# Kernel optimization log

Measured on AMD Instinct MI355X. Metric: run time of the kernel, lower is better.

## Reference

```python
import jax, jax.numpy as jnp
import numpy as np

N, E, R = 50000, 500000, 3
IN, HID, OUT = 128, 128, 128
NEG_SLOPE = 0.2


def setup_inputs() -> dict:
    key = jax.random.key(0)
    ks = jax.random.split(key, 16)
    g = lambda i, shape: jax.random.normal(ks[i], shape, jnp.float32) * 0.1
    return {
        "x": jax.random.normal(ks[0], (N, IN), jnp.float32),
        "edge_index": jax.random.randint(ks[1], (2, E), 0, N, jnp.int32),
        "edge_type": jax.random.randint(ks[2], (E,), 0, R, jnp.int32),
        "edge_attr": jax.random.normal(ks[3], (E, 1), jnp.float32),
        # conv1 params (RGATConv: per-relation weight, q/k/e attention vectors, edge lin, bias)
        "w1": g(4, (R, IN, HID)), "q1": g(5, (HID, 1)), "k1": g(6, (HID, 1)),
        "le1": g(7, (1, HID)), "e1": g(8, (HID, 1)), "b1": jnp.zeros((HID,), jnp.float32),
        # conv2 params
        "w2": g(9, (R, HID, OUT)), "q2": g(10, (OUT, 1)), "k2": g(11, (OUT, 1)),
        "le2": g(12, (1, OUT)), "e2": g(13, (OUT, 1)), "b2": jnp.zeros((OUT,), jnp.float32),
    }


def _rgat_conv(x, src, dst, edge_type, edge_attr, w, q, k, le, e, b):
    """PyG RGATConv: heads=1, dim=1, additive-self-attention, across-relation softmax."""
    n = x.shape[0]
    # Per-relation linear at node level (equiv. to per-edge bmm with w[edge_type])
    xw = jnp.einsum('ni,rio->rno', x, w)            # [R, N, C]
    x_j = xw[edge_type, src]                          # [E, C] transformed source feats
    x_i = xw[edge_type, dst]                          # [E, C] transformed target feats
    # additive attention logits: q(x_i) + k(x_j) + e(lin_edge(edge_attr))
    alpha = x_i @ q + x_j @ k + (edge_attr @ le) @ e  # [E, 1]
    alpha = jax.nn.leaky_relu(alpha, negative_slope=NEG_SLOPE)
    # across-relation softmax over incoming edges of each target node
    amax = jax.ops.segment_max(alpha, dst, num_segments=n)
    amax = jnp.where(jnp.isfinite(amax), amax, 0.0)   # empty segments -> 0
    ex = jnp.exp(alpha - amax[dst])
    denom = jax.ops.segment_sum(ex, dst, num_segments=n)
    alpha = ex / (denom[dst] + 1e-16)
    # weighted scatter-add aggregation, then bias (concat=True, heads=1)
    out = jax.ops.segment_sum(alpha * x_j, dst, num_segments=n)  # [N, C]
    return out + b


def reference(x, edge_index, edge_type, edge_attr,
              w1, q1, k1, le1, e1, b1,
              w2, q2, k2, le2, e2, b2):
    src, dst = edge_index[0], edge_index[1]
    h = jax.nn.relu(_rgat_conv(x, src, dst, edge_type, edge_attr, w1, q1, k1, le1, e1, b1))
    return _rgat_conv(h, src, dst, edge_type, edge_attr, w2, q2, k2, le2, e2, b2)
```

## Files before the change

### kernel.cpp

```cpp
#include <hip/hip_runtime.h>
#include <hip/hip_bf16.h>
#include <math.h>

typedef __bf16 bf16x8 __attribute__((ext_vector_type(8)));
typedef float f32x4 __attribute__((ext_vector_type(4)));

#define CDIM 128

__global__ void sentinel_kernel(float* outf) {
  if (threadIdx.x == 0) outf[0] = 12345.0f;
}

__global__ __launch_bounds__(256) void prep_kernel(
    const float* __restrict__ w1, const float* __restrict__ w2,
    __hip_bfloat16* __restrict__ wt,
    const float* __restrict__ le1, const float* __restrict__ e1,
    const float* __restrict__ le2, const float* __restrict__ e2,
    float* __restrict__ outc, int* __restrict__ deg, int perW, int n) {
  const int b = blockIdx.x;
  const int tid = threadIdx.x;
  if (b < 48) {
    int t = b * 256 + tid;
    if (t >= perW * 2) return;
    const float* w = (t < perW) ? w1 : w2;
    int tt = (t < perW) ? t : t - perW;
    int r = tt >> 11;
    int rem = tt & 2047;
    int kb = rem >> 7;
    int o = rem & 127;
    const float* wr = w + ((size_t)r << 14);
    union { __hip_bfloat16 h[8]; int4 v; } u;
#pragma unroll
    for (int j = 0; j < 8; ++j)
      u.h[j] = __float2bfloat16(wr[(size_t)(kb * 8 + j) * CDIM + o]);
    *reinterpret_cast<int4*>(wt + (size_t)t * 8) = u.v;
  } else if (b == 48) {
    if (tid < 64) {
      float v1 = le1[tid] * e1[tid] + le1[tid + 64] * e1[tid + 64];
      float v2 = le2[tid] * e2[tid] + le2[tid + 64] * e2[tid + 64];
#pragma unroll
      for (int off = 32; off > 0; off >>= 1) {
        v1 += __shfl_xor(v1, off, 64);
        v2 += __shfl_xor(v2, off, 64);
      }
      if (tid == 0) { outc[0] = v1; outc[1] = v2; }
    }
  } else {
    int i = (b - 49) * 256 + tid;
    if (i < n) deg[i] = 0;
  }
}


__global__ __launch_bounds__(256) void hist_kernel(const int* __restrict__ dstv,
                                                   int* __restrict__ deg, int E) {
  int e = blockIdx.x * 256 + threadIdx.x;
  if (e < E) atomicAdd(&deg[dstv[e]], 1);
}

__global__ __launch_bounds__(256) void scan1_kernel(const int* __restrict__ deg,
                                                    int* __restrict__ rowptr,
                                                    int* __restrict__ partials, int n) {
  __shared__ int sh[256];
  int t = threadIdx.x;
  int base = blockIdx.x * 1024;
  int idx = base + t * 4;
  int v[4]; int s = 0;
#pragma unroll
  for (int j = 0; j < 4; ++j) { v[j] = (idx + j < n) ? deg[idx + j] : 0; s += v[j]; }
  sh[t] = s;
  __syncthreads();
  for (int off = 1; off < 256; off <<= 1) {
    int x = (t >= off) ? sh[t - off] : 0;
    __syncthreads();
    sh[t] += x;
    __syncthreads();
  }
  int excl = sh[t] - s;
  if (t == 255) partials[blockIdx.x] = sh[255];
  int run = excl;
#pragma unroll
  for (int j = 0; j < 4; ++j) {
    if (idx + j < n) rowptr[idx + j] = run;
    run += v[j];
  }
}

__global__ __launch_bounds__(256) void scan2_kernel(int* __restrict__ partials, int nb) {
  __shared__ int sh[256];
  int t = threadIdx.x;
  int v = (t < nb) ? partials[t] : 0;
  sh[t] = v;
  __syncthreads();
  for (int off = 1; off < 256; off <<= 1) {
    int x = (t >= off) ? sh[t - off] : 0;
    __syncthreads();
    sh[t] += x;
    __syncthreads();
  }
  if (t < nb) partials[t] = sh[t] - v;
}

__global__ __launch_bounds__(256) void scan3_kernel(int* __restrict__ rowptr,
                                                    int* __restrict__ cursor,
                                                    const int* __restrict__ partials,
                                                    int n, int E) {
  int i = blockIdx.x * 256 + threadIdx.x;
  if (i < n) {
    int v = rowptr[i] + partials[i >> 10];
    rowptr[i] = v;
    cursor[i] = v;
  } else if (i == n) {
    rowptr[n] = E;
  }
}

__global__ __launch_bounds__(256) void scatter_kernel(
    const int* __restrict__ srcv, const int* __restrict__ dstv,
    const int* __restrict__ etype, const float* __restrict__ eattr,
    int* __restrict__ cursor, int2* __restrict__ kattr, int E, int n) {
  int e = blockIdx.x * 256 + threadIdx.x;
  if (e >= E) return;
  int p = atomicAdd(&cursor[dstv[e]], 1);
  kattr[p] = make_int2(etype[e] * n + srcv[e], __float_as_int(eattr[e]));
}

__global__ __launch_bounds__(256) void gemm_xw_kernel(
    const float* __restrict__ xin, const __hip_bfloat16* __restrict__ wt,
    const float* __restrict__ qv, const float* __restrict__ kv,
    __hip_bfloat16* __restrict__ xwout, float* __restrict__ sq, float* __restrict__ sk,
    int n) {
  __shared__ __hip_bfloat16 wlds[16 * 128 * 8];
  __shared__ float qls[128], kls[128];
  const int base = blockIdx.x * 128;
  const int tid = threadIdx.x;
  const int wave = tid >> 6, lane = tid & 63;
  const int quad = lane >> 4, c16 = lane & 15;

  if (tid < 128) qls[tid] = qv[tid];
  else kls[tid - 128] = kv[tid - 128];

  bf16x8 zf;
#pragma unroll
  for (int j = 0; j < 8; ++j) zf[j] = (__bf16)0.0f;

  bf16x8 af[2][4];
#pragma unroll
  for (int h = 0; h < 2; ++h) {
    int m = base + wave * 32 + h * 16 + c16;
#pragma unroll
    for (int ks = 0; ks < 4; ++ks) {
      if (m < n) {
        const float* xp = xin + (size_t)m * CDIM + ks * 32 + quad * 8;
        f32x4 x0 = *reinterpret_cast<const f32x4*>(xp);
        f32x4 x1 = *reinterpret_cast<const f32x4*>(xp + 4);
        bf16x8 a;
#pragma unroll
        for (int j = 0; j < 4; ++j) { a[j] = (__bf16)x0[j]; a[4 + j] = (__bf16)x1[j]; }
        af[h][ks] = a;
      } else {
        af[h][ks] = zf;
      }
    }
  }

  for (int r = 0; r < 3; ++r) {
    if (r) __syncthreads();
    {
      const int4* src = reinterpret_cast<const int4*>(wt + ((size_t)r << 14));
      int4* dst = reinterpret_cast<int4*>(wlds);
      for (int i = tid; i < 2048; i += 256) dst[i] = src[i];
    }
    __syncthreads();

    f32x4 acc[2][8];
#pragma unroll
    for (int h = 0; h < 2; ++h)
#pragma unroll
      for (int ot = 0; ot < 8; ++ot) acc[h][ot] = (f32x4){0.f, 0.f, 0.f, 0.f};

#pragma unroll
    for (int ks = 0; ks < 4; ++ks) {
#pragma unroll
      for (int ot = 0; ot < 8; ++ot) {
        bf16x8 b = *reinterpret_cast<const bf16x8*>(
            &wlds[(((ks * 4 + quad) * 128) + ot * 16 + c16) * 8]);
        acc[0][ot] = __builtin_amdgcn_mfma_f32_16x16x32_bf16(b, af[0][ks], acc[0][ot], 0, 0, 0);
        acc[1][ot] = __builtin_amdgcn_mfma_f32_16x16x32_bf16(b, af[1][ks], acc[1][ot], 0, 0, 0);
      }
    }

#pragma unroll
    for (int h = 0; h < 2; ++h) {
      const int grow = base + wave * 32 + h * 16 + c16;
      const bool ok = grow < n;
      __hip_bfloat16* rp = xwout + (((size_t)r * n + grow) << 7) + quad * 4;
      float s_q = 0.f, s_k = 0.f;
#pragma unroll
      for (int ot = 0; ot < 8; ++ot) {
        f32x4 a = acc[h][ot];
        f32x4 q4 = *reinterpret_cast<const f32x4*>(&qls[ot * 16 + quad * 4]);
        f32x4 k4 = *reinterpret_cast<const f32x4*>(&kls[ot * 16 + quad * 4]);
        s_q += a[0] * q4[0] + a[1] * q4[1] + a[2] * q4[2] + a[3] * q4[3];
        s_k += a[0] * k4[0] + a[1] * k4[1] + a[2] * k4[2] + a[3] * k4[3];
        if (ok) {
          union { __hip_bfloat16 b4[4]; uint2 u; } pk;
#pragma unroll
          for (int t = 0; t < 4; ++t) pk.b4[t] = __float2bfloat16(a[t]);
          *reinterpret_cast<uint2*>(rp + ot * 16) = pk.u;
        }
      }
      s_q += __shfl_xor(s_q, 16, 64);
      s_q += __shfl_xor(s_q, 32, 64);
      s_k += __shfl_xor(s_k, 16, 64);
      s_k += __shfl_xor(s_k, 32, 64);
      if (quad == 0 && ok) {
        sq[(size_t)r * n + grow] = s_q;
        sk[(size_t)r * n + grow] = s_k;
      }
    }
  }
}

__global__ __launch_bounds__(256) void aggregate_kernel(
    const int* __restrict__ rowptr, const int2* __restrict__ kattr,
    const float* __restrict__ sq, const float* __restrict__ sk,
    const __hip_bfloat16* __restrict__ xw, const float* __restrict__ bias,
    const float* __restrict__ cscal, float* __restrict__ out, int n, int do_relu) {
  const int wave = threadIdx.x >> 6, lane = threadIdx.x & 63;
  const int node = blockIdx.x * 4 + wave;
  if (node >= n) return;
  const int g = lane >> 4;
  const int sub = lane & 15;
  const float c = cscal[0];
  const int n2 = n * 2;

  const int start = rowptr[node];
  const int deg = rowptr[node + 1] - start;
  const float s0 = sq[node], s1 = sq[n + node], s2 = sq[n2 + node];

  float acc[8];
#pragma unroll
  for (int t = 0; t < 8; ++t) acc[t] = 0.f;
  float den = 0.f;

  for (int j0 = 0; j0 < deg; j0 += 8) {
    const int j = j0 + (g << 1);
    const bool v0 = j < deg, v1 = j + 1 < deg;
    int2 ka0 = kattr[start + (v0 ? j : 0)];
    int2 ka1 = kattr[start + (v1 ? j + 1 : 0)];
    int kk0 = ka0.x, kk1 = ka1.x;
    float l0 = (kk0 >= n2 ? s2 : (kk0 >= n ? s1 : s0)) + sk[kk0] + c * __int_as_float(ka0.y);
    float l1 = (kk1 >= n2 ? s2 : (kk1 >= n ? s1 : s0)) + sk[kk1] + c * __int_as_float(ka1.y);
    l0 = l0 > 0.f ? l0 : 0.2f * l0;
    l1 = l1 > 0.f ? l1 : 0.2f * l1;
    float w0 = v0 ? __expf(l0) : 0.f;
    float w1 = v1 ? __expf(l1) : 0.f;
    bf16x8 f0 = *reinterpret_cast<const bf16x8*>(xw + ((size_t)kk0 << 7) + sub * 8);
    bf16x8 f1 = *reinterpret_cast<const bf16x8*>(xw + ((size_t)kk1 << 7) + sub * 8);
#pragma unroll
    for (int t = 0; t < 8; ++t) acc[t] += w0 * (float)f0[t] + w1 * (float)f1[t];
    den += w0 + w1;
  }

#pragma unroll
  for (int t = 0; t < 8; ++t) {
    acc[t] += __shfl_xor(acc[t], 16, 64);
    acc[t] += __shfl_xor(acc[t], 32, 64);
  }
  den += __shfl_xor(den, 16, 64);
  den += __shfl_xor(den, 32, 64);

  if (g == 0) {
    float inv = 1.0f / (den + 1e-16f);
    f32x4 b0 = *reinterpret_cast<const f32x4*>(bias + sub * 8);
    f32x4 b1 = *reinterpret_cast<const f32x4*>(bias + sub * 8 + 4);
    f32x4 o0, o1;
#pragma unroll
    for (int t = 0; t < 4; ++t) {
      o0[t] = acc[t] * inv + b0[t];
      o1[t] = acc[4 + t] * inv + b1[t];
    }
    if (do_relu) {
#pragma unroll
      for (int t = 0; t < 4; ++t) {
        o0[t] = fmaxf(o0[t], 0.f);
        o1[t] = fmaxf(o1[t], 0.f);
      }
    }
    float* op = out + (size_t)node * CDIM + sub * 8;
    *reinterpret_cast<f32x4*>(op) = o0;
    *reinterpret_cast<f32x4*>(op + 4) = o1;
  }
}


extern "C" void kernel_launch(void* const* d_in, const int* in_sizes, int n_in,
                              void* d_out, int out_size, void* d_ws, size_t ws_size,
                              hipStream_t stream) {
  const float* x     = (const float*)d_in[0];
  const int*   eidx  = (const int*)d_in[1];
  const int*   etype = (const int*)d_in[2];
  const float* eattr = (const float*)d_in[3];
  const float* w1  = (const float*)d_in[4];
  const float* q1  = (const float*)d_in[5];
  const float* k1  = (const float*)d_in[6];
  const float* le1 = (const float*)d_in[7];
  const float* e1  = (const float*)d_in[8];
  const float* b1  = (const float*)d_in[9];
  const float* w2  = (const float*)d_in[10];
  const float* q2  = (const float*)d_in[11];
  const float* k2  = (const float*)d_in[12];
  const float* le2 = (const float*)d_in[13];
  const float* e2  = (const float*)d_in[14];
  const float* b2  = (const float*)d_in[15];

  const int N = in_sizes[0] / CDIM;
  const int E = in_sizes[2];
  const int R = in_sizes[4] / (CDIM * CDIM);
  const int* srcv = eidx;
  const int* dstv = eidx + E;

  char* p = (char*)d_ws;
  auto alloc = [&](size_t bytes) -> void* {
    void* q = (void*)p;
    p += (bytes + 255) & ~(size_t)255;
    return q;
  };
  float* sq       = (float*)alloc((size_t)R * N * 4);
  float* sk       = (float*)alloc((size_t)R * N * 4);
  int*   deg      = (int*)alloc((size_t)N * 4);
  int*   rowptr   = (int*)alloc((size_t)(N + 1) * 4);
  int*   cursor   = (int*)alloc((size_t)N * 4);
  int*   partials = (int*)alloc(4096);
  int2*  kattr    = (int2*)alloc((size_t)E * 8);
  __hip_bfloat16* wt = (__hip_bfloat16*)alloc((size_t)2 * R * CDIM * CDIM * 2);
  float* cscal    = (float*)alloc(256);
  __hip_bfloat16* xw = (__hip_bfloat16*)alloc((size_t)R * N * CDIM * 2);

  size_t needed = (size_t)(p - (char*)d_ws);
  if (needed > ws_size) {
    sentinel_kernel<<<1, 64, 0, stream>>>((float*)d_out);
    return;
  }

  float* outp = (float*)d_out;
  float* hbuf = outp;

  const int eg = (E + 255) / 256;
  const int nb = (N + 1023) / 1024;
  const int nodes4 = (N + 3) / 4;
  const int perW = R * 2048;
  const int prep_grid = 49 + (N + 255) / 256;

  prep_kernel<<<prep_grid, 256, 0, stream>>>(w1, w2, wt, le1, e1, le2, e2,
                                             cscal, deg, perW, N);

  hist_kernel<<<eg, 256, 0, stream>>>(dstv, deg, E);
  scan1_kernel<<<nb, 256, 0, stream>>>(deg, rowptr, partials, N);
  scan2_kernel<<<1, 256, 0, stream>>>(partials, nb);
  scan3_kernel<<<(N + 1 + 255) / 256, 256, 0, stream>>>(rowptr, cursor, partials, N, E);
  scatter_kernel<<<eg, 256, 0, stream>>>(srcv, dstv, etype, eattr, cursor, kattr, E, N);

  dim3 ggrid((N + 127) / 128);

  gemm_xw_kernel<<<ggrid, 256, 0, stream>>>(x, wt, q1, k1, xw, sq, sk, N);
  aggregate_kernel<<<nodes4, 256, 0, stream>>>(rowptr, kattr, sq, sk, xw, b1,
                                               cscal + 0, hbuf, N, 1);

  gemm_xw_kernel<<<ggrid, 256, 0, stream>>>(hbuf, wt + (size_t)R * CDIM * CDIM,
                                            q2, k2, xw, sq, sk, N);
  aggregate_kernel<<<nodes4, 256, 0, stream>>>(rowptr, kattr, sq, sk, xw, b2,
                                               cscal + 1, outp, N, 0);
}
```

Before: 263.1 us.

## Fold scan2 into scan3, halve GEMM rows per block, unroll aggregate gather 4x

Three separate changes. The second-level prefix scan is folded into scan3 as a per-block wavefront shuffle scan over the partials, which removes one kernel launch. The xW GEMM now gives each block 64 rows instead of 128, with one 16-row tile per wave. This doubles the grid and cuts accumulator registers, at the cost of reloading the weight tiles into LDS twice as often overall. The aggregation loop now has each 16-lane group handle 4 edges per iteration instead of 2, so more independent gathers are in flight. That comes with higher register use and more wasted lanes on low-degree nodes.

```diff
diff --git a/kernel.cpp b/kernel.cpp
--- a/kernel.cpp
+++ b/kernel.cpp
@@ -86,28 +86,26 @@
   }
 }
 
-__global__ __launch_bounds__(256) void scan2_kernel(int* __restrict__ partials, int nb) {
-  __shared__ int sh[256];
-  int t = threadIdx.x;
-  int v = (t < nb) ? partials[t] : 0;
-  sh[t] = v;
-  __syncthreads();
-  for (int off = 1; off < 256; off <<= 1) {
-    int x = (t >= off) ? sh[t - off] : 0;
-    __syncthreads();
-    sh[t] += x;
-    __syncthreads();
-  }
-  if (t < nb) partials[t] = sh[t] - v;
-}
-
 __global__ __launch_bounds__(256) void scan3_kernel(int* __restrict__ rowptr,
                                                     int* __restrict__ cursor,
                                                     const int* __restrict__ partials,
-                                                    int n, int E) {
-  int i = blockIdx.x * 256 + threadIdx.x;
+                                                    int nb, int n, int E) {
+  __shared__ int spfx[64];
+  int t = threadIdx.x;
+  if (t < 64) {
+    int pv = (t < nb) ? partials[t] : 0;
+    int v = pv;
+#pragma unroll
+    for (int off = 1; off < 64; off <<= 1) {
+      int u = __shfl_up(v, off, 64);
+      if (t >= off) v += u;
+    }
+    spfx[t] = v - pv;
+  }
+  __syncthreads();
+  int i = blockIdx.x * 256 + t;
   if (i < n) {
-    int v = rowptr[i] + partials[i >> 10];
+    int v = rowptr[i] + spfx[i >> 10];
     rowptr[i] = v;
     cursor[i] = v;
   } else if (i == n) {
@@ -132,7 +130,7 @@
     int n) {
   __shared__ __hip_bfloat16 wlds[16 * 128 * 8];
   __shared__ float qls[128], kls[128];
-  const int base = blockIdx.x * 128;
+  const int base = blockIdx.x * 64;
   const int tid = threadIdx.x;
   const int wave = tid >> 6, lane = tid & 63;
   const int quad = lane >> 4, c16 = lane & 15;
@@ -144,23 +142,21 @@
 #pragma unroll
   for (int j = 0; j < 8; ++j) zf[j] = (__bf16)0.0f;
 
-  bf16x8 af[2][4];
-#pragma unroll
-  for (int h = 0; h < 2; ++h) {
-    int m = base + wave * 32 + h * 16 + c16;
-#pragma unroll
-    for (int ks = 0; ks < 4; ++ks) {
-      if (m < n) {
-        const float* xp = xin + (size_t)m * CDIM + ks * 32 + quad * 8;
-        f32x4 x0 = *reinterpret_cast<const f32x4*>(xp);
-        f32x4 x1 = *reinterpret_cast<const f32x4*>(xp + 4);
-        bf16x8 a;
-#pragma unroll
-        for (int j = 0; j < 4; ++j) { a[j] = (__bf16)x0[j]; a[4 + j] = (__bf16)x1[j]; }
-        af[h][ks] = a;
-      } else {
-        af[h][ks] = zf;
-      }
+  const int m = base + wave * 16 + c16;
+  const bool ok = m < n;
+  bf16x8 af[4];
+#pragma unroll
+  for (int ks = 0; ks < 4; ++ks) {
+    if (ok) {
+      const float* xp = xin + (size_t)m * CDIM + ks * 32 + quad * 8;
+      f32x4 x0 = *reinterpret_cast<const f32x4*>(xp);
+      f32x4 x1 = *reinterpret_cast<const f32x4*>(xp + 4);
+      bf16x8 a;
+#pragma unroll
+      for (int j = 0; j < 4; ++j) { a[j] = (__bf16)x0[j]; a[4 + j] = (__bf16)x1[j]; }
+      af[ks] = a;
+    } else {
+      af[ks] = zf;
     }
   }
 
@@ -169,15 +165,14 @@
     {
       const int4* src = reinterpret_cast<const int4*>(wt + ((size_t)r << 14));
       int4* dst = reinterpret_cast<int4*>(wlds);
-      for (int i = tid; i < 2048; i += 256) dst[i] = src[i];
+#pragma unroll
+      for (int i = 0; i < 8; ++i) dst[tid + i * 256] = src[tid + i * 256];
     }
     __syncthreads();
 
-    f32x4 acc[2][8];
-#pragma unroll
-    for (int h = 0; h < 2; ++h)
-#pragma unroll
-      for (int ot = 0; ot < 8; ++ot) acc[h][ot] = (f32x4){0.f, 0.f, 0.f, 0.f};
+    f32x4 acc[8];
+#pragma unroll
+    for (int ot = 0; ot < 8; ++ot) acc[ot] = (f32x4){0.f, 0.f, 0.f, 0.f};
 
 #pragma unroll
     for (int ks = 0; ks < 4; ++ks) {
@@ -185,39 +180,33 @@
       for (int ot = 0; ot < 8; ++ot) {
         bf16x8 b = *reinterpret_cast<const bf16x8*>(
             &wlds[(((ks * 4 + quad) * 128) + ot * 16 + c16) * 8]);
-        acc[0][ot] = __builtin_amdgcn_mfma_f32_16x16x32_bf16(b, af[0][ks], acc[0][ot], 0, 0, 0);
-        acc[1][ot] = __builtin_amdgcn_mfma_f32_16x16x32_bf16(b, af[1][ks], acc[1][ot], 0, 0, 0);
+        acc[ot] = __builtin_amdgcn_mfma_f32_16x16x32_bf16(b, af[ks], acc[ot], 0, 0, 0);
       }
     }
 
-#pragma unroll
-    for (int h = 0; h < 2; ++h) {
-      const int grow = base + wave * 32 + h * 16 + c16;
-      const bool ok = grow < n;
-      __hip_bfloat16* rp = xwout + (((size_t)r * n + grow) << 7) + quad * 4;
-      float s_q = 0.f, s_k = 0.f;
-#pragma unroll
-      for (int ot = 0; ot < 8; ++ot) {
-        f32x4 a = acc[h][ot];
-        f32x4 q4 = *reinterpret_cast<const f32x4*>(&qls[ot * 16 + quad * 4]);
-        f32x4 k4 = *reinterpret_cast<const f32x4*>(&kls[ot * 16 + quad * 4]);
-        s_q += a[0] * q4[0] + a[1] * q4[1] + a[2] * q4[2] + a[3] * q4[3];
-        s_k += a[0] * k4[0] + a[1] * k4[1] + a[2] * k4[2] + a[3] * k4[3];
-        if (ok) {
-          union { __hip_bfloat16 b4[4]; uint2 u; } pk;
-#pragma unroll
-          for (int t = 0; t < 4; ++t) pk.b4[t] = __float2bfloat16(a[t]);
-          *reinterpret_cast<uint2*>(rp + ot * 16) = pk.u;
-        }
+    __hip_bfloat16* rp = xwout + (((size_t)r * n + m) << 7) + quad * 4;
+    float s_q = 0.f, s_k = 0.f;
+#pragma unroll
+    for (int ot = 0; ot < 8; ++ot) {
+      f32x4 a = acc[ot];
+      f32x4 q4 = *reinterpret_cast<const f32x4*>(&qls[ot * 16 + quad * 4]);
+      f32x4 k4 = *reinterpret_cast<const f32x4*>(&kls[ot * 16 + quad * 4]);
+      s_q += a[0] * q4[0] + a[1] * q4[1] + a[2] * q4[2] + a[3] * q4[3];
+      s_k += a[0] * k4[0] + a[1] * k4[1] + a[2] * k4[2] + a[3] * k4[3];
+      if (ok) {
+        union { __hip_bfloat16 b4[4]; uint2 u; } pk;
+#pragma unroll
+        for (int t = 0; t < 4; ++t) pk.b4[t] = __float2bfloat16(a[t]);
+        *reinterpret_cast<uint2*>(rp + ot * 16) = pk.u;
       }
-      s_q += __shfl_xor(s_q, 16, 64);
-      s_q += __shfl_xor(s_q, 32, 64);
-      s_k += __shfl_xor(s_k, 16, 64);
-      s_k += __shfl_xor(s_k, 32, 64);
-      if (quad == 0 && ok) {
-        sq[(size_t)r * n + grow] = s_q;
-        sk[(size_t)r * n + grow] = s_k;
-      }
+    }
+    s_q += __shfl_xor(s_q, 16, 64);
+    s_q += __shfl_xor(s_q, 32, 64);
+    s_k += __shfl_xor(s_k, 16, 64);
+    s_k += __shfl_xor(s_k, 32, 64);
+    if (quad == 0 && ok) {
+      sq[(size_t)r * n + m] = s_q;
+      sk[(size_t)r * n + m] = s_k;
     }
   }
 }
@@ -244,23 +233,30 @@
   for (int t = 0; t < 8; ++t) acc[t] = 0.f;
   float den = 0.f;
 
-  for (int j0 = 0; j0 < deg; j0 += 8) {
-    const int j = j0 + (g << 1);
-    const bool v0 = j < deg, v1 = j + 1 < deg;
-    int2 ka0 = kattr[start + (v0 ? j : 0)];
-    int2 ka1 = kattr[start + (v1 ? j + 1 : 0)];
-    int kk0 = ka0.x, kk1 = ka1.x;
-    float l0 = (kk0 >= n2 ? s2 : (kk0 >= n ? s1 : s0)) + sk[kk0] + c * __int_as_float(ka0.y);
-    float l1 = (kk1 >= n2 ? s2 : (kk1 >= n ? s1 : s0)) + sk[kk1] + c * __int_as_float(ka1.y);
-    l0 = l0 > 0.f ? l0 : 0.2f * l0;
-    l1 = l1 > 0.f ? l1 : 0.2f * l1;
-    float w0 = v0 ? __expf(l0) : 0.f;
-    float w1 = v1 ? __expf(l1) : 0.f;
-    bf16x8 f0 = *reinterpret_cast<const bf16x8*>(xw + ((size_t)kk0 << 7) + sub * 8);
-    bf16x8 f1 = *reinterpret_cast<const bf16x8*>(xw + ((size_t)kk1 << 7) + sub * 8);
-#pragma unroll
-    for (int t = 0; t < 8; ++t) acc[t] += w0 * (float)f0[t] + w1 * (float)f1[t];
-    den += w0 + w1;
+  for (int j0 = 0; j0 < deg; j0 += 16) {
+    const int jb = j0 + (g << 2);
+    int2 ka[4];
+#pragma unroll
+    for (int t = 0; t < 4; ++t) {
+      int idx = jb + t;
+      ka[t] = kattr[start + (idx < deg ? idx : 0)];
+    }
+    float w[4];
+    bf16x8 f[4];
+#pragma unroll
+    for (int t = 0; t < 4; ++t) {
+      int kk = ka[t].x;
+      float sv = (kk >= n2) ? s2 : ((kk >= n) ? s1 : s0);
+      float l = sv + sk[kk] + c * __int_as_float(ka[t].y);
+      l = l > 0.f ? l : 0.2f * l;
+      w[t] = (jb + t < deg) ? __expf(l) : 0.f;
+      f[t] = *reinterpret_cast<const bf16x8*>(xw + ((size_t)kk << 7) + sub * 8);
+    }
+#pragma unroll
+    for (int t = 0; t < 8; ++t)
+      acc[t] += w[0] * (float)f[0][t] + w[1] * (float)f[1][t] +
+                w[2] * (float)f[2][t] + w[3] * (float)f[3][t];
+    den += (w[0] + w[1]) + (w[2] + w[3]);
   }
 
 #pragma unroll
@@ -358,11 +354,10 @@
 
   hist_kernel<<<eg, 256, 0, stream>>>(dstv, deg, E);
   scan1_kernel<<<nb, 256, 0, stream>>>(deg, rowptr, partials, N);
-  scan2_kernel<<<1, 256, 0, stream>>>(partials, nb);
-  scan3_kernel<<<(N + 1 + 255) / 256, 256, 0, stream>>>(rowptr, cursor, partials, N, E);
+  scan3_kernel<<<(N + 1 + 255) / 256, 256, 0, stream>>>(rowptr, cursor, partials, nb, N, E);
   scatter_kernel<<<eg, 256, 0, stream>>>(srcv, dstv, etype, eattr, cursor, kattr, E, N);
 
-  dim3 ggrid((N + 127) / 128);
+  dim3 ggrid((N + 63) / 64);
 
   gemm_xw_kernel<<<ggrid, 256, 0, stream>>>(x, wt, q1, k1, xw, sq, sk, N);
   aggregate_kernel<<<nodes4, 256, 0, stream>>>(rowptr, kattr, sq, sk, xw, b1,
```

Measured after the change: 270.5 us. +2.8%, slower.
